# Kernel optimization log

Measured on AMD Instinct MI355X. Metric: run time of the kernel, lower is better.

## Reference

```python
import jax, jax.numpy as jnp
import numpy as np

K = 64          # tagset size (len(tag_to_ix))
START = 62      # start_tag_id
STOP = 63       # stop_tag_id
NEG = -10000.0


def setup_inputs() -> dict:
    key = jax.random.key(0)
    k1, k2, k3 = jax.random.split(key, 3)
    B, T = 1024, 512
    feats = jax.random.normal(k1, (B, T, K), dtype=jnp.float32)
    tags = jax.random.randint(k2, (B, T), 0, K, dtype=jnp.int32)
    # learned transition matrix; transitions[i, j] = score of moving from tag j to tag i
    transitions = jax.random.normal(k3, (K, K), dtype=jnp.float32)
    transitions = transitions.at[START, :].set(NEG).at[:, STOP].set(NEG)
    return {"feats": feats, "tags": tags, "transitions": transitions}


def reference(feats, tags, transitions):
    B, T, _ = feats.shape
    # log_alpha init: -10000 everywhere except start tag (matches torch code; feats[:,0] unused)
    alpha0 = jnp.full((B, K), NEG, dtype=feats.dtype).at[:, START].set(0.0)

    def step(alpha, feat_t):
        # alpha: [B, K]; new_alpha[b, i] = lse_j(transitions[i, j] + alpha[b, j]) + feat_t[b, i]
        new_alpha = jax.nn.logsumexp(transitions[None, :, :] + alpha[:, None, :], axis=-1) + feat_t
        return new_alpha, None

    feats_seq = jnp.transpose(feats[:, 1:, :], (1, 0, 2))  # [T-1, B, K]
    alpha, _ = jax.lax.scan(step, alpha0, feats_seq)
    forward_score = jax.nn.logsumexp(alpha, axis=-1)  # [B]

    # gold path score: sum_t transitions[tags[t], tags[t-1]] + feats[t, tags[t]], t = 1..T-1
    trans_score = transitions[tags[:, 1:], tags[:, :-1]].sum(axis=1)  # [B]
    emit_score = jnp.take_along_axis(feats[:, 1:, :], tags[:, 1:, None], axis=2)[..., 0].sum(axis=1)  # [B]
    gold_score = trans_score + emit_score

    return jnp.mean(forward_score - gold_score)
```

## Files before the change

### kernel.cpp

```cpp
#include <hip/hip_runtime.h>


#define BB 1024
#define TT 512
#define KK 64
#define START_TAG 62

#define RLF(v, l) __uint_as_float((unsigned)__builtin_amdgcn_readlane((int)__float_as_uint(v), (l)))

__global__ __launch_bounds__(64, 1) void crf_forward_kernel(
    const float* __restrict__ feats,
    const int*   __restrict__ tags,
    const float* __restrict__ trans,
    float*       __restrict__ diff)
{
  const int lane = threadIdx.x;
  const int b    = blockIdx.x;

  float4 e4[16];
  {
    const float4* trow = (const float4*)(trans + lane * KK);
    #pragma unroll
    for (int jc = 0; jc < 16; ++jc) {
      float4 tv = trow[jc];
      e4[jc] = make_float4(__expf(tv.x), __expf(tv.y),
                           __expf(tv.z), __expf(tv.w));
    }
  }

  const float* fb = feats + (size_t)b * TT * KK + lane;

  float upf[7];
  #pragma unroll
  for (int d = 0; d < 7; ++d) upf[d] = fb[(size_t)(1 + d) * KK];

  float beta  = (lane == START_TAG) ? 1.0f : 0.0f;
  int   esum  = 0;
  float f_cur = __expf(upf[0]);

  for (int g = 0; g < 73; ++g) {
    #pragma unroll
    for (int d = 0; d < 7; ++d) {
      const int t = 1 + g * 7 + d;

      float4 a0 = {0.f, 0.f, 0.f, 0.f};
      float4 a1 = {0.f, 0.f, 0.f, 0.f};
      #pragma unroll
      for (int jc = 0; jc < 16; jc += 2) {
        a0.x = fmaf(e4[jc].x,     RLF(beta, 4*jc + 0), a0.x);
        a0.y = fmaf(e4[jc].y,     RLF(beta, 4*jc + 1), a0.y);
        a0.z = fmaf(e4[jc].z,     RLF(beta, 4*jc + 2), a0.z);
        a0.w = fmaf(e4[jc].w,     RLF(beta, 4*jc + 3), a0.w);
        a1.x = fmaf(e4[jc + 1].x, RLF(beta, 4*jc + 4), a1.x);
        a1.y = fmaf(e4[jc + 1].y, RLF(beta, 4*jc + 5), a1.y);
        a1.z = fmaf(e4[jc + 1].z, RLF(beta, 4*jc + 6), a1.z);
        a1.w = fmaf(e4[jc + 1].w, RLF(beta, 4*jc + 7), a1.w);
      }
      float z = ((a0.x + a1.x) + (a0.y + a1.y)) +
                ((a0.z + a1.z) + (a0.w + a1.w));

      int tn = t + 7; if (tn > TT - 1) tn = TT - 1;
      upf[d] = fb[(size_t)tn * KK];

      unsigned zb = (unsigned)__builtin_amdgcn_readlane((int)__float_as_uint(z), 0);
      float s = __uint_as_float(0x7F000000u - (zb & 0x7F800000u));
      esum += (int)((zb >> 23) & 0xFFu) - 127;
      beta = (z * f_cur) * s;

      f_cur = __expf((d < 6) ? upf[d + 1] : upf[0]);
    }
  }

  float bs = beta;
  #pragma unroll
  for (int off = 32; off; off >>= 1) bs += __shfl_xor(bs, off);
  float fwd = __logf(bs) + (float)esum * 0.6931471805599453f;

  const int* tg = tags + b * TT;
  float gs = 0.0f;
  for (int tt = 1 + lane; tt < TT; tt += 64) {
    int tc = tg[tt];
    int tp = tg[tt - 1];
    gs += trans[tc * KK + tp]
        + feats[(size_t)b * TT * KK + (size_t)tt * KK + tc];
  }
  #pragma unroll
  for (int off = 32; off; off >>= 1) gs += __shfl_xor(gs, off);

  if (lane == 0) diff[b] = fwd - gs;
}

__global__ __launch_bounds__(1024) void reduce_mean_kernel(
    const float* __restrict__ diff, float* __restrict__ out)
{
  __shared__ float part[16];
  const int tid = threadIdx.x;
  float v = diff[tid];
  #pragma unroll
  for (int off = 32; off; off >>= 1) v += __shfl_xor(v, off);
  if ((tid & 63) == 0) part[tid >> 6] = v;
  __syncthreads();
  if (tid < 16) {
    float s = part[tid];
    #pragma unroll
    for (int off = 8; off; off >>= 1) s += __shfl_xor(s, off);
    if (tid == 0) out[0] = s * (1.0f / 1024.0f);
  }
}

extern "C" void kernel_launch(void* const* d_in, const int* in_sizes, int n_in,
                              void* d_out, int out_size, void* d_ws, size_t ws_size,
                              hipStream_t stream) {
  const float* feats = (const float*)d_in[0];
  const int*   tags  = (const int*)d_in[1];
  const float* trans = (const float*)d_in[2];
  float* out  = (float*)d_out;
  float* diff = (float*)d_ws;

  crf_forward_kernel<<<dim3(BB), dim3(64), 0, stream>>>(feats, tags, trans, diff);
  reduce_mean_kernel<<<dim3(1), dim3(1024), 0, stream>>>(diff, out);
}
```

Before: 284.0 us.

## Split CRF recursion into concurrent forward and backward halves per sequence

Each block now runs two wavefronts. One computes the forward alpha recursion over t=1..255 and the other computes a backward beta recursion over t=511..256 using the transposed transition matrix. The two are joined at the midpoint with a dot product through shared memory. The goal is to halve the serial dependency chain length, which dominates this latency-bound scan, at the cost of doubling register and wave usage per sequence and adding a block sync.

Result: faster. 260.0 us (-8.5%).

```diff
diff --git a/kernel.cpp b/kernel.cpp
--- a/kernel.cpp
+++ b/kernel.cpp
@@ -8,86 +8,153 @@
 
 #define RLF(v, l) __uint_as_float((unsigned)__builtin_amdgcn_readlane((int)__float_as_uint(v), (l)))
 
-__global__ __launch_bounds__(64, 1) void crf_forward_kernel(
+__global__ __launch_bounds__(128, 2) void crf_fwdbwd_kernel(
     const float* __restrict__ feats,
     const int*   __restrict__ tags,
     const float* __restrict__ trans,
     float*       __restrict__ diff)
 {
-  const int lane = threadIdx.x;
+  const int lane = threadIdx.x & 63;
+  const int wv   = threadIdx.x >> 6;
   const int b    = blockIdx.x;
 
-  float4 e4[16];
-  {
-    const float4* trow = (const float4*)(trans + lane * KK);
-    #pragma unroll
-    for (int jc = 0; jc < 16; ++jc) {
-      float4 tv = trow[jc];
-      e4[jc] = make_float4(__expf(tv.x), __expf(tv.y),
-                           __expf(tv.z), __expf(tv.w));
-    }
-  }
+  __shared__ float ysh[KK];
+  __shared__ float gs_sh;
+  __shared__ int   esumB_sh;
 
   const float* fb = feats + (size_t)b * TT * KK + lane;
 
-  float upf[7];
-  #pragma unroll
-  for (int d = 0; d < 7; ++d) upf[d] = fb[(size_t)(1 + d) * KK];
+  float beta = 0.0f;
+  int   esumA = 0;
 
-  float beta  = (lane == START_TAG) ? 1.0f : 0.0f;
-  int   esum  = 0;
-  float f_cur = __expf(upf[0]);
+  if (wv == 0) {
+    float4 e4[16];
+    {
+      const float4* trow = (const float4*)(trans + lane * KK);
+      #pragma unroll
+      for (int jc = 0; jc < 16; ++jc) {
+        float4 tv = trow[jc];
+        e4[jc] = make_float4(__expf(tv.x), __expf(tv.y),
+                             __expf(tv.z), __expf(tv.w));
+      }
+    }
 
-  for (int g = 0; g < 73; ++g) {
+    float upf[5];
     #pragma unroll
-    for (int d = 0; d < 7; ++d) {
-      const int t = 1 + g * 7 + d;
+    for (int d = 0; d < 5; ++d) upf[d] = fb[(size_t)(1 + d) * KK];
 
-      float4 a0 = {0.f, 0.f, 0.f, 0.f};
-      float4 a1 = {0.f, 0.f, 0.f, 0.f};
+    beta = (lane == START_TAG) ? 1.0f : 0.0f;
+    float f_cur = __expf(upf[0]);
+
+    for (int g = 0; g < 51; ++g) {
       #pragma unroll
-      for (int jc = 0; jc < 16; jc += 2) {
-        a0.x = fmaf(e4[jc].x,     RLF(beta, 4*jc + 0), a0.x);
-        a0.y = fmaf(e4[jc].y,     RLF(beta, 4*jc + 1), a0.y);
-        a0.z = fmaf(e4[jc].z,     RLF(beta, 4*jc + 2), a0.z);
-        a0.w = fmaf(e4[jc].w,     RLF(beta, 4*jc + 3), a0.w);
-        a1.x = fmaf(e4[jc + 1].x, RLF(beta, 4*jc + 4), a1.x);
-        a1.y = fmaf(e4[jc + 1].y, RLF(beta, 4*jc + 5), a1.y);
-        a1.z = fmaf(e4[jc + 1].z, RLF(beta, 4*jc + 6), a1.z);
-        a1.w = fmaf(e4[jc + 1].w, RLF(beta, 4*jc + 7), a1.w);
+      for (int d = 0; d < 5; ++d) {
+        const int t = 1 + g * 5 + d;
+
+        float4 a0 = {0.f, 0.f, 0.f, 0.f};
+        float4 a1 = {0.f, 0.f, 0.f, 0.f};
+        #pragma unroll
+        for (int jc = 0; jc < 16; jc += 2) {
+          a0.x = fmaf(e4[jc].x,     RLF(beta, 4*jc + 0), a0.x);
+          a0.y = fmaf(e4[jc].y,     RLF(beta, 4*jc + 1), a0.y);
+          a0.z = fmaf(e4[jc].z,     RLF(beta, 4*jc + 2), a0.z);
+          a0.w = fmaf(e4[jc].w,     RLF(beta, 4*jc + 3), a0.w);
+          a1.x = fmaf(e4[jc + 1].x, RLF(beta, 4*jc + 4), a1.x);
+          a1.y = fmaf(e4[jc + 1].y, RLF(beta, 4*jc + 5), a1.y);
+          a1.z = fmaf(e4[jc + 1].z, RLF(beta, 4*jc + 6), a1.z);
+          a1.w = fmaf(e4[jc + 1].w, RLF(beta, 4*jc + 7), a1.w);
+        }
+        float z = ((a0.x + a1.x) + (a0.y + a1.y)) +
+                  ((a0.z + a1.z) + (a0.w + a1.w));
+
+        int tn = t + 5; if (tn > 255) tn = 255;
+        upf[d] = fb[(size_t)tn * KK];
+
+        unsigned zb = (unsigned)__builtin_amdgcn_readlane((int)__float_as_uint(z), 0);
+        float s = __uint_as_float(0x7F000000u - (zb & 0x7F800000u));
+        esumA += (int)((zb >> 23) & 0xFFu) - 127;
+        beta = (z * f_cur) * s;
+
+        f_cur = __expf(upf[(d + 1 < 5) ? d + 1 : 0]);
       }
-      float z = ((a0.x + a1.x) + (a0.y + a1.y)) +
-                ((a0.z + a1.z) + (a0.w + a1.w));
+    }
+  } else {
+    float4 et4[16];
+    #pragma unroll
+    for (int jc = 0; jc < 16; ++jc) {
+      et4[jc].x = __expf(trans[(4*jc + 0) * KK + lane]);
+      et4[jc].y = __expf(trans[(4*jc + 1) * KK + lane]);
+      et4[jc].z = __expf(trans[(4*jc + 2) * KK + lane]);
+      et4[jc].w = __expf(trans[(4*jc + 3) * KK + lane]);
+    }
 
-      int tn = t + 7; if (tn > TT - 1) tn = TT - 1;
-      upf[d] = fb[(size_t)tn * KK];
+    float upf[4];
+    #pragma unroll
+    for (int d = 0; d < 4; ++d) upf[d] = fb[(size_t)(511 - d) * KK];
 
-      unsigned zb = (unsigned)__builtin_amdgcn_readlane((int)__float_as_uint(z), 0);
-      float s = __uint_as_float(0x7F000000u - (zb & 0x7F800000u));
-      esum += (int)((zb >> 23) & 0xFFu) - 127;
-      beta = (z * f_cur) * s;
+    float y = 1.0f;
+    int esum = 0;
+    float f_cur = __expf(upf[0]);
 
-      f_cur = __expf((d < 6) ? upf[d + 1] : upf[0]);
+    for (int g = 0; g < 64; ++g) {
+      #pragma unroll
+      for (int d = 0; d < 4; ++d) {
+        const int t = 511 - (g * 4 + d);
+
+        float w = y * f_cur;
+        float4 a0 = {0.f, 0.f, 0.f, 0.f};
+        float4 a1 = {0.f, 0.f, 0.f, 0.f};
+        #pragma unroll
+        for (int jc = 0; jc < 16; jc += 2) {
+          a0.x = fmaf(et4[jc].x,     RLF(w, 4*jc + 0), a0.x);
+          a0.y = fmaf(et4[jc].y,     RLF(w, 4*jc + 1), a0.y);
+          a0.z = fmaf(et4[jc].z,     RLF(w, 4*jc + 2), a0.z);
+          a0.w = fmaf(et4[jc].w,     RLF(w, 4*jc + 3), a0.w);
+          a1.x = fmaf(et4[jc + 1].x, RLF(w, 4*jc + 4), a1.x);
+          a1.y = fmaf(et4[jc + 1].y, RLF(w, 4*jc + 5), a1.y);
+          a1.z = fmaf(et4[jc + 1].z, RLF(w, 4*jc + 6), a1.z);
+          a1.w = fmaf(et4[jc + 1].w, RLF(w, 4*jc + 7), a1.w);
+        }
+        float z = ((a0.x + a1.x) + (a0.y + a1.y)) +
+                  ((a0.z + a1.z) + (a0.w + a1.w));
+
+        int tn = t - 4; if (tn < 256) tn = 256;
+        upf[d] = fb[(size_t)tn * KK];
+
+        unsigned zb = (unsigned)__builtin_amdgcn_readlane((int)__float_as_uint(z), 0);
+        float s = __uint_as_float(0x7F000000u - (zb & 0x7F800000u));
+        esum += (int)((zb >> 23) & 0xFFu) - 127;
+        y = z * s;
+
+        f_cur = __expf(upf[(d + 1) & 3]);
+      }
     }
+
+    ysh[lane] = y;
+    if (lane == 0) esumB_sh = esum;
+
+    const int* tg = tags + b * TT;
+    float gs = 0.0f;
+    for (int tt = 1 + lane; tt < TT; tt += 64) {
+      int tc = tg[tt];
+      int tp = tg[tt - 1];
+      gs += trans[tc * KK + tp]
+          + feats[(size_t)b * TT * KK + (size_t)tt * KK + tc];
+    }
+    #pragma unroll
+    for (int off = 32; off; off >>= 1) gs += __shfl_xor(gs, off);
+    if (lane == 0) gs_sh = gs;
   }
 
-  float bs = beta;
-  #pragma unroll
-  for (int off = 32; off; off >>= 1) bs += __shfl_xor(bs, off);
-  float fwd = __logf(bs) + (float)esum * 0.6931471805599453f;
+  __syncthreads();
 
-  const int* tg = tags + b * TT;
-  float gs = 0.0f;
-  for (int tt = 1 + lane; tt < TT; tt += 64) {
-    int tc = tg[tt];
-    int tp = tg[tt - 1];
-    gs += trans[tc * KK + tp]
-        + feats[(size_t)b * TT * KK + (size_t)tt * KK + tc];
+  if (wv == 0) {
+    float p = beta * ysh[lane];
+    #pragma unroll
+    for (int off = 32; off; off >>= 1) p += __shfl_xor(p, off);
+    float fwd = __logf(p) + (float)(esumA + esumB_sh) * 0.6931471805599453f;
+    if (lane == 0) diff[b] = fwd - gs_sh;
   }
-  #pragma unroll
-  for (int off = 32; off; off >>= 1) gs += __shfl_xor(gs, off);
-
-  if (lane == 0) diff[b] = fwd - gs;
 }
 
 __global__ __launch_bounds__(1024) void reduce_mean_kernel(
@@ -117,6 +184,6 @@
   float* out  = (float*)d_out;
   float* diff = (float*)d_ws;
 
-  crf_forward_kernel<<<dim3(BB), dim3(64), 0, stream>>>(feats, tags, trans, diff);
+  crf_fwdbwd_kernel<<<dim3(BB), dim3(128), 0, stream>>>(feats, tags, trans, diff);
   reduce_mean_kernel<<<dim3(1), dim3(1024), 0, stream>>>(diff, out);
 }
```

## Run forward and backward CRF recursions concurrently and meet in the middle

Applied to the files above, without the earlier changes.

Splits the 511-step sequential forward recursion into a forward pass over steps 1..255 and a backward pass over steps 511..256 using transposed exp-transitions. The two chains are interleaved inside one wavefront and combined at the middle with a dot product. This halves the serial dependency chain length, so the two chains can hide each other's readlane/FMA latency. In exchange it doubles register use for the transition matrix and does twice the independent work per step, which may pressure VGPRs.

Measured after the change: 277.5 us. -2.3%, faster.

```diff
diff --git a/kernel.cpp b/kernel.cpp
--- a/kernel.cpp
+++ b/kernel.cpp
@@ -8,7 +8,7 @@
 
 #define RLF(v, l) __uint_as_float((unsigned)__builtin_amdgcn_readlane((int)__float_as_uint(v), (l)))
 
-__global__ __launch_bounds__(64, 1) void crf_forward_kernel(
+__global__ __launch_bounds__(64, 1) void crf_fused_kernel(
     const float* __restrict__ feats,
     const int*   __restrict__ tags,
     const float* __restrict__ trans,
@@ -27,54 +27,113 @@
                            __expf(tv.z), __expf(tv.w));
     }
   }
+  float4 et4[16];
+  #pragma unroll
+  for (int jc = 0; jc < 16; ++jc) {
+    et4[jc].x = __expf(trans[(4*jc + 0) * KK + lane]);
+    et4[jc].y = __expf(trans[(4*jc + 1) * KK + lane]);
+    et4[jc].z = __expf(trans[(4*jc + 2) * KK + lane]);
+    et4[jc].w = __expf(trans[(4*jc + 3) * KK + lane]);
+  }
 
   const float* fb = feats + (size_t)b * TT * KK + lane;
 
-  float upf[7];
+  float upfA[5];
+  float upfB[5];
   #pragma unroll
-  for (int d = 0; d < 7; ++d) upf[d] = fb[(size_t)(1 + d) * KK];
+  for (int d = 0; d < 5; ++d) {
+    upfA[d] = fb[(size_t)(1 + d) * KK];
+    upfB[d] = fb[(size_t)(511 - d) * KK];
+  }
 
-  float beta  = (lane == START_TAG) ? 1.0f : 0.0f;
-  int   esum  = 0;
-  float f_cur = __expf(upf[0]);
+  float beta = (lane == START_TAG) ? 1.0f : 0.0f;
+  float y    = 1.0f;
+  int   esumA = 0, esumB = 0;
+  float fA = __expf(upfA[0]);
+  float fB = __expf(upfB[0]);
 
-  for (int g = 0; g < 73; ++g) {
+  for (int g = 0; g < 51; ++g) {
     #pragma unroll
-    for (int d = 0; d < 7; ++d) {
-      const int t = 1 + g * 7 + d;
+    for (int d = 0; d < 5; ++d) {
+      const int tA = 1 + g * 5 + d;
+      const int tB = 511 - (g * 5 + d);
+
+      float w = y * fB;
 
       float4 a0 = {0.f, 0.f, 0.f, 0.f};
       float4 a1 = {0.f, 0.f, 0.f, 0.f};
+      float4 c0 = {0.f, 0.f, 0.f, 0.f};
+      float4 c1 = {0.f, 0.f, 0.f, 0.f};
       #pragma unroll
       for (int jc = 0; jc < 16; jc += 2) {
-        a0.x = fmaf(e4[jc].x,     RLF(beta, 4*jc + 0), a0.x);
-        a0.y = fmaf(e4[jc].y,     RLF(beta, 4*jc + 1), a0.y);
-        a0.z = fmaf(e4[jc].z,     RLF(beta, 4*jc + 2), a0.z);
-        a0.w = fmaf(e4[jc].w,     RLF(beta, 4*jc + 3), a0.w);
-        a1.x = fmaf(e4[jc + 1].x, RLF(beta, 4*jc + 4), a1.x);
-        a1.y = fmaf(e4[jc + 1].y, RLF(beta, 4*jc + 5), a1.y);
-        a1.z = fmaf(e4[jc + 1].z, RLF(beta, 4*jc + 6), a1.z);
-        a1.w = fmaf(e4[jc + 1].w, RLF(beta, 4*jc + 7), a1.w);
+        a0.x = fmaf(e4[jc].x,      RLF(beta, 4*jc + 0), a0.x);
+        c0.x = fmaf(et4[jc].x,     RLF(w,    4*jc + 0), c0.x);
+        a0.y = fmaf(e4[jc].y,      RLF(beta, 4*jc + 1), a0.y);
+        c0.y = fmaf(et4[jc].y,     RLF(w,    4*jc + 1), c0.y);
+        a0.z = fmaf(e4[jc].z,      RLF(beta, 4*jc + 2), a0.z);
+        c0.z = fmaf(et4[jc].z,     RLF(w,    4*jc + 2), c0.z);
+        a0.w = fmaf(e4[jc].w,      RLF(beta, 4*jc + 3), a0.w);
+        c0.w = fmaf(et4[jc].w,     RLF(w,    4*jc + 3), c0.w);
+        a1.x = fmaf(e4[jc + 1].x,  RLF(beta, 4*jc + 4), a1.x);
+        c1.x = fmaf(et4[jc + 1].x, RLF(w,    4*jc + 4), c1.x);
+        a1.y = fmaf(e4[jc + 1].y,  RLF(beta, 4*jc + 5), a1.y);
+        c1.y = fmaf(et4[jc + 1].y, RLF(w,    4*jc + 5), c1.y);
+        a1.z = fmaf(e4[jc + 1].z,  RLF(beta, 4*jc + 6), a1.z);
+        c1.z = fmaf(et4[jc + 1].z, RLF(w,    4*jc + 6), c1.z);
+        a1.w = fmaf(e4[jc + 1].w,  RLF(beta, 4*jc + 7), a1.w);
+        c1.w = fmaf(et4[jc + 1].w, RLF(w,    4*jc + 7), c1.w);
       }
-      float z = ((a0.x + a1.x) + (a0.y + a1.y)) +
-                ((a0.z + a1.z) + (a0.w + a1.w));
+      float zA = ((a0.x + a1.x) + (a0.y + a1.y)) +
+                 ((a0.z + a1.z) + (a0.w + a1.w));
+      float zB = ((c0.x + c1.x) + (c0.y + c1.y)) +
+                 ((c0.z + c1.z) + (c0.w + c1.w));
 
-      int tn = t + 7; if (tn > TT - 1) tn = TT - 1;
-      upf[d] = fb[(size_t)tn * KK];
+      int tnA = tA + 5; if (tnA > 255) tnA = 255;
+      int tnB = tB - 5; if (tnB < 256) tnB = 256;
+      upfA[d] = fb[(size_t)tnA * KK];
+      upfB[d] = fb[(size_t)tnB * KK];
 
-      unsigned zb = (unsigned)__builtin_amdgcn_readlane((int)__float_as_uint(z), 0);
-      float s = __uint_as_float(0x7F000000u - (zb & 0x7F800000u));
-      esum += (int)((zb >> 23) & 0xFFu) - 127;
-      beta = (z * f_cur) * s;
+      unsigned zbA = (unsigned)__builtin_amdgcn_readlane((int)__float_as_uint(zA), 0);
+      unsigned zbB = (unsigned)__builtin_amdgcn_readlane((int)__float_as_uint(zB), 0);
+      float sA = __uint_as_float(0x7F000000u - (zbA & 0x7F800000u));
+      float sB = __uint_as_float(0x7F000000u - (zbB & 0x7F800000u));
+      esumA += (int)((zbA >> 23) & 0xFFu) - 127;
+      esumB += (int)((zbB >> 23) & 0xFFu) - 127;
+      beta = (zA * fA) * sA;
+      y    = zB * sB;
 
-      f_cur = __expf((d < 6) ? upf[d + 1] : upf[0]);
+      fA = __expf(upfA[(d + 1 < 5) ? d + 1 : 0]);
+      fB = __expf(upfB[(d + 1 < 5) ? d + 1 : 0]);
     }
   }
 
-  float bs = beta;
+  {
+    float w = y * fB;
+    float4 c0 = {0.f, 0.f, 0.f, 0.f};
+    float4 c1 = {0.f, 0.f, 0.f, 0.f};
+    #pragma unroll
+    for (int jc = 0; jc < 16; jc += 2) {
+      c0.x = fmaf(et4[jc].x,     RLF(w, 4*jc + 0), c0.x);
+      c0.y = fmaf(et4[jc].y,     RLF(w, 4*jc + 1), c0.y);
+      c0.z = fmaf(et4[jc].z,     RLF(w, 4*jc + 2), c0.z);
+      c0.w = fmaf(et4[jc].w,     RLF(w, 4*jc + 3), c0.w);
+      c1.x = fmaf(et4[jc + 1].x, RLF(w, 4*jc + 4), c1.x);
+      c1.y = fmaf(et4[jc + 1].y, RLF(w, 4*jc + 5), c1.y);
+      c1.z = fmaf(et4[jc + 1].z, RLF(w, 4*jc + 6), c1.z);
+      c1.w = fmaf(et4[jc + 1].w, RLF(w, 4*jc + 7), c1.w);
+    }
+    float zB = ((c0.x + c1.x) + (c0.y + c1.y)) +
+               ((c0.z + c1.z) + (c0.w + c1.w));
+    unsigned zbB = (unsigned)__builtin_amdgcn_readlane((int)__float_as_uint(zB), 0);
+    float sB = __uint_as_float(0x7F000000u - (zbB & 0x7F800000u));
+    esumB += (int)((zbB >> 23) & 0xFFu) - 127;
+    y = zB * sB;
+  }
+
+  float p = beta * y;
   #pragma unroll
-  for (int off = 32; off; off >>= 1) bs += __shfl_xor(bs, off);
-  float fwd = __logf(bs) + (float)esum * 0.6931471805599453f;
+  for (int off = 32; off; off >>= 1) p += __shfl_xor(p, off);
+  float fwd = __logf(p) + (float)(esumA + esumB) * 0.6931471805599453f;
 
   const int* tg = tags + b * TT;
   float gs = 0.0f;
@@ -117,6 +176,6 @@
   float* out  = (float*)d_out;
   float* diff = (float*)d_ws;
 
-  crf_forward_kernel<<<dim3(BB), dim3(64), 0, stream>>>(feats, tags, trans, diff);
+  crf_fused_kernel<<<dim3(BB), dim3(64), 0, stream>>>(feats, tags, trans, diff);
   reduce_mean_kernel<<<dim3(1), dim3(1024), 0, stream>>>(diff, out);
 }
```

## Run CRF forward recursion on MFMA with bidirectional chains over batch tiles

Applied to the files above, without the earlier changes.

Replaces the per-sequence readlane FMA matvec with 16x16x32 fp16 MFMAs over a tile of 16 sequences. fp32 precision is emulated with hi/lo splits, using three products per pair. Each block runs a forward chain and a backward chain in two waves that meet in the middle, which halves the serial dependency length. The two halves are joined through shared memory with a dot product. Only 64 blocks are launched, so fewer CUs are used, and the split-fp16 approximation may change accuracy slightly.

Result: slower. 423.5 us (+49.1%).

```diff
diff --git a/kernel.cpp b/kernel.cpp
--- a/kernel.cpp
+++ b/kernel.cpp
@@ -5,89 +5,223 @@
 #define TT 512
 #define KK 64
 #define START_TAG 62
-
-#define RLF(v, l) __uint_as_float((unsigned)__builtin_amdgcn_readlane((int)__float_as_uint(v), (l)))
-
-__global__ __launch_bounds__(64, 1) void crf_forward_kernel(
+#define NBLK 64
+#define GB 16
+
+typedef _Float16 f16;
+typedef f16   f16x8 __attribute__((ext_vector_type(8)));
+typedef float f32x4 __attribute__((ext_vector_type(4)));
+
+union W8 { f16x8 v; f16 e[8]; };
+
+#define MFMA16(A, B, C) __builtin_amdgcn_mfma_f32_16x16x32_f16((A), (B), (C), 0, 0, 0)
+
+__device__ __forceinline__ f32x4 exp4(f32x4 u) {
+  f32x4 r; r.x = __expf(u.x); r.y = __expf(u.y); r.z = __expf(u.z); r.w = __expf(u.w);
+  return r;
+}
+
+__device__ __forceinline__ unsigned umaxu(unsigned a, unsigned b) { return a > b ? a : b; }
+
+__device__ __forceinline__ void normalize(const f32x4 (&q)[4], f32x4 (&v)[4], int& esum) {
+  unsigned mb = 0u;
+  #pragma unroll
+  for (int tau = 0; tau < 4; ++tau) {
+    mb = umaxu(mb, __float_as_uint(q[tau].x));
+    mb = umaxu(mb, __float_as_uint(q[tau].y));
+    mb = umaxu(mb, __float_as_uint(q[tau].z));
+    mb = umaxu(mb, __float_as_uint(q[tau].w));
+  }
+  mb = umaxu(mb, (unsigned)__shfl_xor((int)mb, 16));
+  mb = umaxu(mb, (unsigned)__shfl_xor((int)mb, 32));
+  esum += (int)(mb >> 23) - 127;
+  const float s = __uint_as_float(0x7F000000u - (mb & 0x7F800000u));
+  #pragma unroll
+  for (int tau = 0; tau < 4; ++tau) v[tau] = q[tau] * s;
+}
+
+__device__ __forceinline__ void pack_w(const f32x4 (&v)[4], W8 (&whi)[2], W8 (&wlo)[2]) {
+  #pragma unroll
+  for (int S = 0; S < 2; ++S) {
+    #pragma unroll
+    for (int c = 0; c < 2; ++c) {
+      const f32x4 t = v[2 * S + c];
+      const f16 h0 = (f16)t.x, h1 = (f16)t.y, h2 = (f16)t.z, h3 = (f16)t.w;
+      whi[S].e[4 * c + 0] = h0;
+      whi[S].e[4 * c + 1] = h1;
+      whi[S].e[4 * c + 2] = h2;
+      whi[S].e[4 * c + 3] = h3;
+      wlo[S].e[4 * c + 0] = (f16)(t.x - (float)h0);
+      wlo[S].e[4 * c + 1] = (f16)(t.y - (float)h1);
+      wlo[S].e[4 * c + 2] = (f16)(t.z - (float)h2);
+      wlo[S].e[4 * c + 3] = (f16)(t.w - (float)h3);
+    }
+  }
+}
+
+__device__ __forceinline__ void mfma_step(const W8 (&Ehi)[4][2], const W8 (&Elo)[4][2],
+                                          const W8 (&whi)[2], const W8 (&wlo)[2],
+                                          f32x4 (&acc)[4]) {
+  #pragma unroll
+  for (int tau = 0; tau < 4; ++tau) {
+    f32x4 a = {0.f, 0.f, 0.f, 0.f};
+    a = MFMA16(Ehi[tau][0].v, whi[0].v, a);
+    a = MFMA16(Ehi[tau][1].v, whi[1].v, a);
+    a = MFMA16(Elo[tau][0].v, whi[0].v, a);
+    a = MFMA16(Elo[tau][1].v, whi[1].v, a);
+    a = MFMA16(Ehi[tau][0].v, wlo[0].v, a);
+    a = MFMA16(Ehi[tau][1].v, wlo[1].v, a);
+    acc[tau] = a;
+  }
+}
+
+template <int DIR>
+__device__ __forceinline__ void run_chain(const float* __restrict__ feats,
+                                          const float* __restrict__ trans,
+                                          int blk, int lane,
+                                          f32x4 (&v)[4], int& esum) {
+  const int m = lane & 15;
+  const int h = lane >> 4;
+
+  W8 Ehi[4][2], Elo[4][2];
+  #pragma unroll
+  for (int tau = 0; tau < 4; ++tau)
+    #pragma unroll
+    for (int S = 0; S < 2; ++S)
+      #pragma unroll
+      for (int e = 0; e < 8; ++e) {
+        const int kk = 32 * S + 16 * (e >> 2) + 4 * h + (e & 3);
+        const int row = 16 * tau + m;
+        const float val = __expf(DIR ? trans[kk * KK + row] : trans[row * KK + kk]);
+        const f16 hi = (f16)val;
+        Ehi[tau][S].e[e] = hi;
+        Elo[tau][S].e[e] = (f16)(val - (float)hi);
+      }
+
+  const float* fB = feats + (size_t)(blk * GB + m) * TT * KK + 4 * h;
+
+  W8 whi[2], wlo[2];
+  f32x4 uN[4], g[4];
+  esum = 0;
+
+  if (DIR == 0) {
+    f32x4 vv[4];
+    #pragma unroll
+    for (int tau = 0; tau < 4; ++tau) vv[tau] = (f32x4){0.f, 0.f, 0.f, 0.f};
+    if (h == 3) vv[3].z = 1.0f;
+    pack_w(vv, whi, wlo);
+    #pragma unroll
+    for (int tau = 0; tau < 4; ++tau) {
+      f32x4 u0 = *(const f32x4*)(fB + (size_t)1 * KK + 16 * tau);
+      uN[tau]  = *(const f32x4*)(fB + (size_t)2 * KK + 16 * tau);
+      g[tau] = exp4(u0);
+    }
+  } else {
+    f32x4 q[4];
+    #pragma unroll
+    for (int tau = 0; tau < 4; ++tau) {
+      f32x4 u0 = *(const f32x4*)(fB + (size_t)511 * KK + 16 * tau);
+      uN[tau]  = *(const f32x4*)(fB + (size_t)510 * KK + 16 * tau);
+      q[tau] = exp4(u0);
+    }
+    normalize(q, v, esum);
+    pack_w(v, whi, wlo);
+    #pragma unroll
+    for (int tau = 0; tau < 4; ++tau) {
+      g[tau] = exp4(uN[tau]);
+      uN[tau] = *(const f32x4*)(fB + (size_t)509 * KK + 16 * tau);
+    }
+  }
+
+  for (int i = 0; i < 255; ++i) {
+    f32x4 acc[4];
+    mfma_step(Ehi, Elo, whi, wlo, acc);
+
+    const int tf = DIR ? (508 - i) : (3 + i);
+    f32x4 uF[4];
+    #pragma unroll
+    for (int tau = 0; tau < 4; ++tau)
+      uF[tau] = *(const f32x4*)(fB + (size_t)tf * KK + 16 * tau);
+
+    f32x4 q[4];
+    #pragma unroll
+    for (int tau = 0; tau < 4; ++tau) q[tau] = acc[tau] * g[tau];
+    normalize(q, v, esum);
+    pack_w(v, whi, wlo);
+
+    #pragma unroll
+    for (int tau = 0; tau < 4; ++tau) { g[tau] = exp4(uN[tau]); uN[tau] = uF[tau]; }
+  }
+
+  if (DIR == 1) {
+    f32x4 acc[4];
+    mfma_step(Ehi, Elo, whi, wlo, acc);
+    normalize(acc, v, esum);
+  }
+}
+
+__global__ __launch_bounds__(128, 1) void crf_mfma_kernel(
     const float* __restrict__ feats,
     const int*   __restrict__ tags,
     const float* __restrict__ trans,
     float*       __restrict__ diff)
 {
-  const int lane = threadIdx.x;
-  const int b    = blockIdx.x;
-
-  float4 e4[16];
-  {
-    const float4* trow = (const float4*)(trans + lane * KK);
-    #pragma unroll
-    for (int jc = 0; jc < 16; ++jc) {
-      float4 tv = trow[jc];
-      e4[jc] = make_float4(__expf(tv.x), __expf(tv.y),
-                           __expf(tv.z), __expf(tv.w));
-    }
-  }
-
-  const float* fb = feats + (size_t)b * TT * KK + lane;
-
-  float upf[7];
-  #pragma unroll
-  for (int d = 0; d < 7; ++d) upf[d] = fb[(size_t)(1 + d) * KK];
-
-  float beta  = (lane == START_TAG) ? 1.0f : 0.0f;
-  int   esum  = 0;
-  float f_cur = __expf(upf[0]);
-
-  for (int g = 0; g < 73; ++g) {
-    #pragma unroll
-    for (int d = 0; d < 7; ++d) {
-      const int t = 1 + g * 7 + d;
-
-      float4 a0 = {0.f, 0.f, 0.f, 0.f};
-      float4 a1 = {0.f, 0.f, 0.f, 0.f};
-      #pragma unroll
-      for (int jc = 0; jc < 16; jc += 2) {
-        a0.x = fmaf(e4[jc].x,     RLF(beta, 4*jc + 0), a0.x);
-        a0.y = fmaf(e4[jc].y,     RLF(beta, 4*jc + 1), a0.y);
-        a0.z = fmaf(e4[jc].z,     RLF(beta, 4*jc + 2), a0.z);
-        a0.w = fmaf(e4[jc].w,     RLF(beta, 4*jc + 3), a0.w);
-        a1.x = fmaf(e4[jc + 1].x, RLF(beta, 4*jc + 4), a1.x);
-        a1.y = fmaf(e4[jc + 1].y, RLF(beta, 4*jc + 5), a1.y);
-        a1.z = fmaf(e4[jc + 1].z, RLF(beta, 4*jc + 6), a1.z);
-        a1.w = fmaf(e4[jc + 1].w, RLF(beta, 4*jc + 7), a1.w);
-      }
-      float z = ((a0.x + a1.x) + (a0.y + a1.y)) +
-                ((a0.z + a1.z) + (a0.w + a1.w));
-
-      int tn = t + 7; if (tn > TT - 1) tn = TT - 1;
-      upf[d] = fb[(size_t)tn * KK];
-
-      unsigned zb = (unsigned)__builtin_amdgcn_readlane((int)__float_as_uint(z), 0);
-      float s = __uint_as_float(0x7F000000u - (zb & 0x7F800000u));
-      esum += (int)((zb >> 23) & 0xFFu) - 127;
-      beta = (z * f_cur) * s;
-
-      f_cur = __expf((d < 6) ? upf[d + 1] : upf[0]);
-    }
-  }
-
-  float bs = beta;
-  #pragma unroll
-  for (int off = 32; off; off >>= 1) bs += __shfl_xor(bs, off);
-  float fwd = __logf(bs) + (float)esum * 0.6931471805599453f;
-
-  const int* tg = tags + b * TT;
-  float gs = 0.0f;
-  for (int tt = 1 + lane; tt < TT; tt += 64) {
-    int tc = tg[tt];
-    int tp = tg[tt - 1];
-    gs += trans[tc * KK + tp]
-        + feats[(size_t)b * TT * KK + (size_t)tt * KK + tc];
-  }
-  #pragma unroll
-  for (int off = 32; off; off >>= 1) gs += __shfl_xor(gs, off);
-
-  if (lane == 0) diff[b] = fwd - gs;
+  const int lane = threadIdx.x & 63;
+  const int wv   = threadIdx.x >> 6;
+  const int blk  = blockIdx.x;
+  const int m = lane & 15;
+  const int h = lane >> 4;
+
+  __shared__ float ysh[KK][GB];
+  __shared__ int   esum_sh[GB];
+
+  f32x4 v[4];
+  int esum;
+
+  if (wv == 1) {
+    run_chain<1>(feats, trans, blk, lane, v, esum);
+    #pragma unroll
+    for (int tau = 0; tau < 4; ++tau) {
+      ysh[16 * tau + 4 * h + 0][m] = v[tau].x;
+      ysh[16 * tau + 4 * h + 1][m] = v[tau].y;
+      ysh[16 * tau + 4 * h + 2][m] = v[tau].z;
+      ysh[16 * tau + 4 * h + 3][m] = v[tau].w;
+    }
+    if (lane < 16) esum_sh[lane] = esum;
+    __syncthreads();
+  } else {
+    run_chain<0>(feats, trans, blk, lane, v, esum);
+
+    const int bglob = blk * GB + m;
+    const int* tg = tags + bglob * TT;
+    const float* fg = feats + (size_t)bglob * TT * KK;
+    float gs = 0.f;
+    #pragma unroll 8
+    for (int tt = 1 + h; tt < TT; tt += 4) {
+      const int tc = tg[tt];
+      const int tp = tg[tt - 1];
+      gs += trans[tc * KK + tp] + fg[(size_t)tt * KK + tc];
+    }
+    gs += __shfl_xor(gs, 16);
+    gs += __shfl_xor(gs, 32);
+
+    __syncthreads();
+
+    float p = 0.f;
+    #pragma unroll
+    for (int tau = 0; tau < 4; ++tau) {
+      p += v[tau].x * ysh[16 * tau + 4 * h + 0][m];
+      p += v[tau].y * ysh[16 * tau + 4 * h + 1][m];
+      p += v[tau].z * ysh[16 * tau + 4 * h + 2][m];
+      p += v[tau].w * ysh[16 * tau + 4 * h + 3][m];
+    }
+    p += __shfl_xor(p, 16);
+    p += __shfl_xor(p, 32);
+
+    if (lane < 16)
+      diff[blk * GB + lane] =
+          __logf(p) + (float)(esum + esum_sh[lane]) * 0.6931471805599453f - gs;
+  }
 }
 
 __global__ __launch_bounds__(1024) void reduce_mean_kernel(
@@ -117,6 +251,6 @@
   float* out  = (float*)d_out;
   float* diff = (float*)d_ws;
 
-  crf_forward_kernel<<<dim3(BB), dim3(64), 0, stream>>>(feats, tags, trans, diff);
+  crf_mfma_kernel<<<dim3(NBLK), dim3(128), 0, stream>>>(feats, tags, trans, diff);
   reduce_mean_kernel<<<dim3(1), dim3(1024), 0, stream>>>(diff, out);
 }
```
